# Performance work log

Measured on AMD Instinct MI355X. Metric: run time of the kernel, lower is better.

The kernel has to match this reference:

```python
import jax, jax.numpy as jnp
import numpy as np

B, C, N, K, C_OUT = 16, 64, 2048, 3, 64


def setup_inputs() -> dict:
    key = jax.random.key(0)
    k1, k2, k3 = jax.random.split(key, 3)
    x = jax.random.normal(k1, (B, C, N), dtype=jnp.float32)
    # Conv1d params: weight [out_ch, in_ch, K], bias [out_ch]
    fan_in = C * K
    bound = 1.0 / np.sqrt(fan_in)
    W = jax.random.uniform(k2, (C_OUT, C, K), dtype=jnp.float32, minval=-bound, maxval=bound)
    b = jax.random.uniform(k3, (C_OUT,), dtype=jnp.float32, minval=-bound, maxval=bound)
    return {"x": x, "W": W, "b": b}


def reference(x, W, b):
    # x: [B, C, N]
    # pairwise squared-distance matrix over the length dim: [B, N, N]
    norm_sq = jnp.sum(x * x, axis=1, keepdims=True)              # [B, 1, N]
    dot = jnp.einsum('bcn,bcm->bnm', x, x)                       # [B, N, N]
    dist = norm_sq + jnp.swapaxes(norm_sq, 1, 2) - 2.0 * dot     # [B, N, N]
    # K smallest distances per point (self included, dist=0)
    _, idx = jax.lax.top_k(-dist, K)                             # [B, N, K]
    # gather neighbors: prime[b, c, n*K + k] = x[b, c, idx[b, n, k]]
    idx_flat = idx.reshape(B, 1, N * K)
    prime = jnp.take_along_axis(x, jnp.broadcast_to(idx_flat, (B, C, N * K)), axis=2)
    # Conv1d(kernel=K, stride=K, padding=0) -> [B, C_OUT, N]
    out = jax.lax.conv_general_dilated(
        prime, W, window_strides=(K,), padding='VALID',
        dimension_numbers=('NCH', 'OIH', 'NCH'))
    out = out + b[None, :, None]
    return jax.nn.relu(out)
```

## Files before the change

kernel.cpp:

```cpp
#include <hip/hip_runtime.h>
#include <float.h>

#define BB 16
#define CC 64
#define NN 2048
#define KNN 3
#define COUT 64
#define SPL 8

typedef _Float16 half8 __attribute__((ext_vector_type(8)));
typedef float f32x16 __attribute__((ext_vector_type(16)));

__global__ __launch_bounds__(256) void k_prep(const float* __restrict__ x,
                                              uint4* __restrict__ xe,
                                              unsigned* __restrict__ anc) {
    __shared__ float t[64][65];
    __shared__ float nsh[64];
    const int b = blockIdx.x;
    const int n0 = blockIdx.y * 64;
    const int tid = threadIdx.x;
    const int ln = tid & 63, g = tid >> 6;
#pragma unroll
    for (int i = 0; i < 16; ++i) {
        const int c = g + 4 * i;
        t[c][ln] = x[((size_t)b * CC + c) * NN + n0 + ln];
    }
    __syncthreads();
    if (tid < 64) {
        float s = 0.f;
#pragma unroll
        for (int c = 0; c < 64; ++c) s = fmaf(t[c][tid], t[c][tid], s);
        nsh[tid] = s;
    }
#pragma unroll
    for (int i = 0; i < 4; ++i) {
        const int cid = tid + 256 * i;
        const int lane = cid & 63;
        const int kblk = (cid >> 6) & 7;
        const int ctl = cid >> 9;
        const int m = ctl * 32 + (lane & 31);
        const int khalf = (lane >> 5) * 8;
        union { uint4 v; _Float16 h[8]; } pk;
#pragma unroll
        for (int j = 0; j < 8; ++j) {
            const int kg = kblk * 16 + khalf + j;
            const int ch = kg & 63;
            const float f = t[ch][m];
            const _Float16 hi = (_Float16)f;
            pk.h[j] = (kg < 64) ? hi : (_Float16)(f - (float)hi);
        }
        const int ct = (n0 >> 5) + ctl;
        xe[((size_t)(b * 64 + ct) * 8 + kblk) * 64 + lane] = pk.v;
    }
    __syncthreads();
    if (tid < 64) {
        const int ctl = tid >> 5, l = tid & 31;
        const int ct = (n0 >> 5) + ctl;
        const float h = -0.5f * nsh[ctl * 32 + l];
        const _Float16 a0 = (_Float16)h;
        const _Float16 a1 = (_Float16)(h - (float)a0);
        union { unsigned u; _Float16 hh[2]; } cu;
        cu.hh[0] = a0; cu.hh[1] = a1;
        anc[(size_t)(b * 64 + ct) * 32 + l] = cu.u;
    }
}

__global__ __launch_bounds__(256) void k_wprep(const float* __restrict__ W,
                                               uint4* __restrict__ Wf) {
    const int tid = threadIdx.x;
#pragma unroll
    for (int i = 0; i < 6; ++i) {
        const int id = tid + 256 * i;
        const int l = id & 63;
        const int kb = (id >> 6) & 3;
        const int ct2 = (id >> 8) & 1;
        const int kk = id >> 9;
        const int co = ct2 * 32 + (l & 31);
        union { uint4 v; _Float16 h[8]; } pk;
#pragma unroll
        for (int j = 0; j < 8; ++j) {
            const int c = kb * 16 + 8 * (l >> 5) + j;
            pk.h[j] = (_Float16)W[(co * CC + c) * KNN + kk];
        }
        Wf[id] = pk.v;
    }
}

__global__ __launch_bounds__(256, 2) void k_top3(const half8* __restrict__ xe,
                                                 const unsigned* __restrict__ anc,
                                                 uint4* __restrict__ pk) {
    const int tid = threadIdx.x;
    const int lane = tid & 63;
    const int wq = blockIdx.x * 4 + (tid >> 6);
    const int qgA = wq * 2, qgB = wq * 2 + 1;
    const int s = blockIdx.y;
    const int b = blockIdx.z;

    half8 bqA[8], bqB[8];
#pragma unroll
    for (int kb = 0; kb < 8; ++kb) {
        bqA[kb] = xe[((size_t)(b * 64 + qgA) * 8 + kb) * 64 + lane];
        bqB[kb] = xe[((size_t)(b * 64 + qgB) * 8 + kb) * 64 + lane];
    }
    half8 bnc = {};
    if (lane < 32) { bnc[0] = (_Float16)1.0f; bnc[1] = (_Float16)1.0f; }

    float kA0 = -FLT_MAX, kA1 = -FLT_MAX, kA2 = -FLT_MAX;
    float kB0 = -FLT_MAX, kB1 = -FLT_MAX, kB2 = -FLT_MAX;
    int iA0 = -1, iA1 = -1, iA2 = -1;
    int iB0 = -1, iB1 = -1, iB2 = -1;
    const int hi4 = (lane >> 5) * 4;

    constexpr int TILES = NN / 32 / SPL;
    const int ct0 = s * TILES;
    for (int t = 0; t < TILES; ++t) {
        const int ct = ct0 + t;
        half8 af[8];
#pragma unroll
        for (int kb = 0; kb < 8; ++kb)
            af[kb] = xe[((size_t)(b * 64 + ct) * 8 + kb) * 64 + lane];
        half8 av = {};
        {
            union { unsigned u; _Float16 hh[2]; } cu;
            cu.u = anc[(size_t)(b * 64 + ct) * 32 + (lane & 31)];
            av[0] = cu.hh[0]; av[1] = cu.hh[1];
        }
        f32x16 accA = {}, accB = {};
#pragma unroll
        for (int kb = 0; kb < 8; ++kb) {
            accA = __builtin_amdgcn_mfma_f32_32x32x16_f16(af[kb], bqA[kb], accA, 0, 0, 0);
            accB = __builtin_amdgcn_mfma_f32_32x32x16_f16(af[kb], bqB[kb], accB, 0, 0, 0);
        }
#pragma unroll
        for (int kb = 0; kb < 8; ++kb) {
            accA = __builtin_amdgcn_mfma_f32_32x32x16_f16(af[kb], bqA[(kb + 4) & 7], accA, 0, 0, 0);
            accB = __builtin_amdgcn_mfma_f32_32x32x16_f16(af[kb], bqB[(kb + 4) & 7], accB, 0, 0, 0);
        }
        accA = __builtin_amdgcn_mfma_f32_32x32x16_f16(av, bnc, accA, 0, 0, 0);
        accB = __builtin_amdgcn_mfma_f32_32x32x16_f16(av, bnc, accB, 0, 0, 0);

        const int mbase = t * 32 + hi4;
#pragma unroll
        for (int j = 0; j < 16; ++j) {
            const float a = accA[j];
            if (__any(a > kA2)) {
                const int m = mbase + (j & 3) + 8 * (j >> 2);
                const bool g0 = a > kA0, g1 = a > kA1, g2 = a > kA2;
                kA2 = g1 ? kA1 : (g2 ? a : kA2); iA2 = g1 ? iA1 : (g2 ? m : iA2);
                kA1 = g0 ? kA0 : (g1 ? a : kA1); iA1 = g0 ? iA0 : (g1 ? m : iA1);
                kA0 = g0 ? a : kA0;              iA0 = g0 ? m : iA0;
            }
        }
#pragma unroll
        for (int j = 0; j < 16; ++j) {
            const float a = accB[j];
            if (__any(a > kB2)) {
                const int m = mbase + (j & 3) + 8 * (j >> 2);
                const bool g0 = a > kB0, g1 = a > kB1, g2 = a > kB2;
                kB2 = g1 ? kB1 : (g2 ? a : kB2); iB2 = g1 ? iB1 : (g2 ? m : iB2);
                kB1 = g0 ? kB0 : (g1 ? a : kB1); iB1 = g0 ? iB0 : (g1 ? m : iB1);
                kB0 = g0 ? a : kB0;              iB0 = g0 ? m : iB0;
            }
        }
    }

#pragma unroll
    for (int grp = 0; grp < 2; ++grp) {
        float K0 = grp ? kB0 : kA0, K1 = grp ? kB1 : kA1, K2 = grp ? kB2 : kA2;
        int I0 = grp ? iB0 : iA0, I1 = grp ? iB1 : iA1, I2 = grp ? iB2 : iA2;
        const float ok0 = __shfl_xor(K0, 32), ok1 = __shfl_xor(K1, 32), ok2 = __shfl_xor(K2, 32);
        const int oi0 = __shfl_xor(I0, 32), oi1 = __shfl_xor(I1, 32), oi2 = __shfl_xor(I2, 32);
        const float ck[3] = {ok0, ok1, ok2};
        const int cix[3] = {oi0, oi1, oi2};
#pragma unroll
        for (int r = 0; r < 3; ++r) {
            const float c = ck[r]; const int ci = cix[r];
            const bool b0 = (c > K0) || (c == K0 && ci < I0);
            const bool b1 = (c > K1) || (c == K1 && ci < I1);
            const bool b2 = (c > K2) || (c == K2 && ci < I2);
            K2 = b1 ? K1 : (b2 ? c : K2); I2 = b1 ? I1 : (b2 ? ci : I2);
            K1 = b0 ? K0 : (b1 ? c : K1); I1 = b0 ? I0 : (b1 ? ci : I1);
            K0 = b0 ? c : K0;             I0 = b0 ? ci : I0;
        }
        if (lane < 32) {
            const int q = (grp ? qgB : qgA) * 32 + lane;
            uint4 v;
            v.x = __float_as_uint(K0);
            v.y = __float_as_uint(K1);
            v.z = __float_as_uint(K2);
            v.w = (unsigned)I0 | ((unsigned)I1 << 8) | ((unsigned)I2 << 16);
            pk[((size_t)b * SPL + s) * NN + q] = v;
        }
    }
}

__global__ __launch_bounds__(256) void k_merge(const uint4* __restrict__ pk,
                                               int* __restrict__ fi) {
    const int t = blockIdx.x * 256 + threadIdx.x;
    if (t >= BB * NN) return;
    const int b = t / NN, n = t % NN;
    float dv[3 * SPL]; int iv[3 * SPL];
#pragma unroll
    for (int s = 0; s < SPL; ++s) {
        const uint4 v = pk[((size_t)b * SPL + s) * NN + n];
        dv[s * 3 + 0] = __uint_as_float(v.x);
        dv[s * 3 + 1] = __uint_as_float(v.y);
        dv[s * 3 + 2] = __uint_as_float(v.z);
        iv[s * 3 + 0] = (int)(v.w & 255u) + s * 256;
        iv[s * 3 + 1] = (int)((v.w >> 8) & 255u) + s * 256;
        iv[s * 3 + 2] = (int)((v.w >> 16) & 255u) + s * 256;
    }
    float bd = FLT_MAX; int bi = -1;
#pragma unroll
    for (int r = 0; r < 3; ++r) {
        float ck = -FLT_MAX; int ci = 0x7fffffff;
#pragma unroll
        for (int j = 0; j < 3 * SPL; ++j) {
            const bool after_prev = (dv[j] < bd) || (dv[j] == bd && iv[j] > bi);
            const bool better = (dv[j] > ck) || (dv[j] == ck && iv[j] < ci);
            if (after_prev && better) { ck = dv[j]; ci = iv[j]; }
        }
        fi[(size_t)t * 3 + r] = ci;
        bd = ck; bi = ci;
    }
}

__global__ __launch_bounds__(256) void k_conv(const uint4* __restrict__ xe,
                                              const uint4* __restrict__ Wf,
                                              const int* __restrict__ fi,
                                              const float* __restrict__ bias,
                                              float* __restrict__ out) {
    __shared__ float ot[64][65];
    const int b = blockIdx.y;
    const int n0 = blockIdx.x * 64;
    const int tid = threadIdx.x;
    const int l = tid & 63;
    const int w = tid >> 6;
    const int mt = w >> 1, ct2 = w & 1;
    const int p31 = l & 31, kh = l >> 5;
    const int npt = n0 + mt * 32 + p31;

    f32x16 acc = {};
    const uint4* xb = xe + (size_t)b * 64 * 8 * 64;
    const int fbase3 = (b * NN + npt) * KNN;
#pragma unroll
    for (int kk = 0; kk < KNN; ++kk) {
        const int src = fi[fbase3 + kk];
        const uint4* ap = xb + (size_t)(src >> 5) * 512 + (src & 31) + 32 * kh;
        uint4 af[4], bw[4];
#pragma unroll
        for (int kb = 0; kb < 4; ++kb) af[kb] = ap[(size_t)kb * 64];
#pragma unroll
        for (int kb = 0; kb < 4; ++kb) bw[kb] = Wf[((kk * 2 + ct2) * 4 + kb) * 64 + l];
#pragma unroll
        for (int kb = 0; kb < 4; ++kb) {
            union { uint4 v; half8 h; } ua, ub;
            ua.v = af[kb]; ub.v = bw[kb];
            acc = __builtin_amdgcn_mfma_f32_32x32x16_f16(ua.h, ub.h, acc, 0, 0, 0);
        }
    }
    const int co = ct2 * 32 + p31;
    const float bv = bias[co];
#pragma unroll
    for (int j = 0; j < 16; ++j) {
        const int pt = mt * 32 + (j & 3) + 8 * (j >> 2) + 4 * kh;
        ot[co][pt] = fmaxf(acc[j] + bv, 0.f);
    }
    __syncthreads();
#pragma unroll
    for (int i = 0; i < 16; ++i) {
        const int v = tid + 256 * i;
        const int co2 = v >> 6, col = v & 63;
        out[((size_t)(b * COUT + co2)) * NN + n0 + col] = ot[co2][col];
    }
}

extern "C" void kernel_launch(void* const* d_in, const int* in_sizes, int n_in,
                              void* d_out, int out_size, void* d_ws, size_t ws_size,
                              hipStream_t stream) {
    const float* x = (const float*)d_in[0];
    const float* W = (const float*)d_in[1];
    const float* bias = (const float*)d_in[2];
    float* out = (float*)d_out;

    char* ws = (char*)d_ws;
    uint4* xe = (uint4*)(ws);
    unsigned* anc = (unsigned*)(ws + 8388608);
    uint4* Wf = (uint4*)(ws + 8519680);
    uint4* pk = (uint4*)(ws + 8544256);
    int* fi = (int*)(ws + 12738560);

    k_prep<<<dim3(BB, NN / 64), 256, 0, stream>>>(x, xe, anc);
    k_wprep<<<1, 256, 0, stream>>>(W, Wf);
    k_top3<<<dim3(8, SPL, BB), 256, 0, stream>>>((const half8*)xe, anc, pk);
    k_merge<<<(BB * NN + 255) / 256, 256, 0, stream>>>(pk, fi);
    k_conv<<<dim3(NN / 64, BB), 256, 0, stream>>>(xe, Wf, fi, bias, out);
}
```

Measured before the change: 81.54 us.

## Stage candidate tiles through double-buffered LDS with async global-to-LDS loads in top3

The top-3 kernel now loads each candidate tile of fp16 features into a shared double buffer using global_load_lds, with the four waves each fetching two k-blocks and prefetching the next tile while computing the current one. Before, every wave loaded the full tile from global memory itself. The MFMA loop is split into halves that read from LDS to reduce register pressure, and launch bounds are raised to 4 blocks per CU. In exchange it adds a block-wide barrier per tile and relies on async LDS loads being complete at that barrier.

```diff
diff --git a/kernel.cpp b/kernel.cpp
--- a/kernel.cpp
+++ b/kernel.cpp
@@ -10,6 +10,14 @@
 
 typedef _Float16 half8 __attribute__((ext_vector_type(8)));
 typedef float f32x16 __attribute__((ext_vector_type(16)));
+
+union u4h8 { uint4 v; half8 h; };
+
+__device__ __forceinline__ void gl_lds16(const void* g, void* l) {
+    __builtin_amdgcn_global_load_lds(
+        (const __attribute__((address_space(1))) unsigned*)g,
+        (__attribute__((address_space(3))) unsigned*)l, 16, 0, 0);
+}
 
 __global__ __launch_bounds__(256) void k_prep(const float* __restrict__ x,
                                               uint4* __restrict__ xe,
@@ -86,12 +94,14 @@
     }
 }
 
-__global__ __launch_bounds__(256, 2) void k_top3(const half8* __restrict__ xe,
+__global__ __launch_bounds__(256, 4) void k_top3(const uint4* __restrict__ xe,
                                                  const unsigned* __restrict__ anc,
                                                  uint4* __restrict__ pk) {
+    __shared__ uint4 buf[2][8][64];
     const int tid = threadIdx.x;
     const int lane = tid & 63;
-    const int wq = blockIdx.x * 4 + (tid >> 6);
+    const int w = tid >> 6;
+    const int wq = blockIdx.x * 4 + w;
     const int qgA = wq * 2, qgB = wq * 2 + 1;
     const int s = blockIdx.y;
     const int b = blockIdx.z;
@@ -99,8 +109,10 @@
     half8 bqA[8], bqB[8];
 #pragma unroll
     for (int kb = 0; kb < 8; ++kb) {
-        bqA[kb] = xe[((size_t)(b * 64 + qgA) * 8 + kb) * 64 + lane];
-        bqB[kb] = xe[((size_t)(b * 64 + qgB) * 8 + kb) * 64 + lane];
+        u4h8 tA, tB;
+        tA.v = xe[((size_t)(b * 64 + qgA) * 8 + kb) * 64 + lane];
+        tB.v = xe[((size_t)(b * 64 + qgB) * 8 + kb) * 64 + lane];
+        bqA[kb] = tA.h; bqB[kb] = tB.h;
     }
     half8 bnc = {};
     if (lane < 32) { bnc[0] = (_Float16)1.0f; bnc[1] = (_Float16)1.0f; }
@@ -113,31 +125,55 @@
 
     constexpr int TILES = NN / 32 / SPL;
     const int ct0 = s * TILES;
+    const uint4* xb = xe + (size_t)(b * 64) * 512;
+    const int kb0 = 2 * w, kb1 = 2 * w + 1;
+
+    gl_lds16(xb + ((size_t)ct0 * 8 + kb0) * 64 + lane, &buf[0][kb0][0]);
+    gl_lds16(xb + ((size_t)ct0 * 8 + kb1) * 64 + lane, &buf[0][kb1][0]);
+    __syncthreads();
+
+#pragma unroll
     for (int t = 0; t < TILES; ++t) {
+        const int bi = t & 1;
         const int ct = ct0 + t;
-        half8 af[8];
-#pragma unroll
-        for (int kb = 0; kb < 8; ++kb)
-            af[kb] = xe[((size_t)(b * 64 + ct) * 8 + kb) * 64 + lane];
-        half8 av = {};
+        if (t + 1 < TILES) {
+            gl_lds16(xb + ((size_t)(ct + 1) * 8 + kb0) * 64 + lane, &buf[bi ^ 1][kb0][0]);
+            gl_lds16(xb + ((size_t)(ct + 1) * 8 + kb1) * 64 + lane, &buf[bi ^ 1][kb1][0]);
+        }
+        const unsigned av_u = anc[(size_t)(b * 64 + ct) * 32 + (lane & 31)];
+
+        f32x16 accA = {}, accB = {};
         {
+            u4h8 ah[4];
+#pragma unroll
+            for (int kb = 0; kb < 4; ++kb) ah[kb].v = buf[bi][kb][lane];
+#pragma unroll
+            for (int kb = 0; kb < 4; ++kb) {
+                accA = __builtin_amdgcn_mfma_f32_32x32x16_f16(ah[kb].h, bqA[kb], accA, 0, 0, 0);
+                accB = __builtin_amdgcn_mfma_f32_32x32x16_f16(ah[kb].h, bqB[kb], accB, 0, 0, 0);
+            }
+#pragma unroll
+            for (int kb = 0; kb < 4; ++kb) {
+                accA = __builtin_amdgcn_mfma_f32_32x32x16_f16(ah[kb].h, bqA[kb + 4], accA, 0, 0, 0);
+                accB = __builtin_amdgcn_mfma_f32_32x32x16_f16(ah[kb].h, bqB[kb + 4], accB, 0, 0, 0);
+            }
+        }
+        {
+            u4h8 al[4];
+#pragma unroll
+            for (int kb = 0; kb < 4; ++kb) al[kb].v = buf[bi][4 + kb][lane];
+#pragma unroll
+            for (int kb = 0; kb < 4; ++kb) {
+                accA = __builtin_amdgcn_mfma_f32_32x32x16_f16(al[kb].h, bqA[kb], accA, 0, 0, 0);
+                accB = __builtin_amdgcn_mfma_f32_32x32x16_f16(al[kb].h, bqB[kb], accB, 0, 0, 0);
+            }
+            half8 av = {};
             union { unsigned u; _Float16 hh[2]; } cu;
-            cu.u = anc[(size_t)(b * 64 + ct) * 32 + (lane & 31)];
+            cu.u = av_u;
             av[0] = cu.hh[0]; av[1] = cu.hh[1];
-        }
-        f32x16 accA = {}, accB = {};
-#pragma unroll
-        for (int kb = 0; kb < 8; ++kb) {
-            accA = __builtin_amdgcn_mfma_f32_32x32x16_f16(af[kb], bqA[kb], accA, 0, 0, 0);
-            accB = __builtin_amdgcn_mfma_f32_32x32x16_f16(af[kb], bqB[kb], accB, 0, 0, 0);
-        }
-#pragma unroll
-        for (int kb = 0; kb < 8; ++kb) {
-            accA = __builtin_amdgcn_mfma_f32_32x32x16_f16(af[kb], bqA[(kb + 4) & 7], accA, 0, 0, 0);
-            accB = __builtin_amdgcn_mfma_f32_32x32x16_f16(af[kb], bqB[(kb + 4) & 7], accB, 0, 0, 0);
-        }
-        accA = __builtin_amdgcn_mfma_f32_32x32x16_f16(av, bnc, accA, 0, 0, 0);
-        accB = __builtin_amdgcn_mfma_f32_32x32x16_f16(av, bnc, accB, 0, 0, 0);
+            accA = __builtin_amdgcn_mfma_f32_32x32x16_f16(av, bnc, accA, 0, 0, 0);
+            accB = __builtin_amdgcn_mfma_f32_32x32x16_f16(av, bnc, accB, 0, 0, 0);
+        }
 
         const int mbase = t * 32 + hi4;
 #pragma unroll
@@ -162,6 +198,7 @@
                 kB0 = g0 ? a : kB0;              iB0 = g0 ? m : iB0;
             }
         }
+        __syncthreads();
     }
 
 #pragma unroll
@@ -254,7 +291,7 @@
         for (int kb = 0; kb < 4; ++kb) bw[kb] = Wf[((kk * 2 + ct2) * 4 + kb) * 64 + l];
 #pragma unroll
         for (int kb = 0; kb < 4; ++kb) {
-            union { uint4 v; half8 h; } ua, ub;
+            u4h8 ua, ub;
             ua.v = af[kb]; ub.v = bw[kb];
             acc = __builtin_amdgcn_mfma_f32_32x32x16_f16(ua.h, ub.h, acc, 0, 0, 0);
         }
@@ -292,7 +329,7 @@
 
     k_prep<<<dim3(BB, NN / 64), 256, 0, stream>>>(x, xe, anc);
     k_wprep<<<1, 256, 0, stream>>>(W, Wf);
-    k_top3<<<dim3(8, SPL, BB), 256, 0, stream>>>((const half8*)xe, anc, pk);
+    k_top3<<<dim3(8, SPL, BB), 256, 0, stream>>>(xe, anc, pk);
     k_merge<<<(BB * NN + 255) / 256, 256, 0, stream>>>(pk, fi);
     k_conv<<<dim3(NN / 64, BB), 256, 0, stream>>>(xe, Wf, fi, bias, out);
 }
```

Measured after the change: 82.12 us. No clear change (+0.7%).
